# Kernel optimization log

Measured on AMD Instinct MI355X. Metric: run time of the kernel, lower is better.

Reference implementation:

```python
import jax, jax.numpy as jnp
import numpy as np

B, S, H = 2, 2048, 2048
NH, NKV = 16, 4
HD = H // NH          # 128
N_REP = NH // NKV     # 4


def _rotate_half(x):
    x1, x2 = x[..., : x.shape[-1] // 2], x[..., x.shape[-1] // 2 :]
    return jnp.concatenate((-x2, x1), axis=-1)


def setup_inputs() -> dict:
    key = jax.random.key(0)
    ks = jax.random.split(key, 5)
    hidden_states = jax.random.normal(ks[0], (B, S, H), dtype=jnp.float32)
    # true rotary tables [max_seq_len, head_dim]
    inv_freq = 1.0 / (10000.0 ** (np.arange(0, HD, 2, dtype=np.float32) / HD))
    t = np.arange(S, dtype=np.float32)
    freqs = np.outer(t, inv_freq)                    # [S, HD/2]
    emb = np.concatenate([freqs, freqs], axis=-1)    # [S, HD]
    cos = jnp.asarray(np.cos(emb))
    sin = jnp.asarray(np.sin(emb))
    Wq = jax.random.normal(ks[1], (H, NH * HD), dtype=jnp.float32) * 0.02
    Wk = jax.random.normal(ks[2], (H, NKV * HD), dtype=jnp.float32) * 0.02
    Wv = jax.random.normal(ks[3], (H, NKV * HD), dtype=jnp.float32) * 0.02
    Wo = jax.random.normal(ks[4], (NH * HD, H), dtype=jnp.float32) * 0.02
    attention_mask = jnp.ones((B, S), dtype=jnp.float32)  # 1 = keep
    return {"hidden_states": hidden_states, "cos": cos, "sin": sin,
            "Wq": Wq, "Wk": Wk, "Wv": Wv, "Wo": Wo,
            "attention_mask": attention_mask}


def reference(hidden_states, cos, sin, Wq, Wk, Wv, Wo, attention_mask):
    # Decoder self-attention: is_causal=True, use_rope=True, no cache, eval (dropout off).
    x = hidden_states
    b, s, _ = x.shape
    q = jnp.einsum('bsh,hd->bsd', x, Wq).reshape(b, s, NH, HD).transpose(0, 2, 1, 3)   # [b,nh,s,hd]
    k = jnp.einsum('bsh,hd->bsd', x, Wk).reshape(b, s, NKV, HD)
    v = jnp.einsum('bsh,hd->bsd', x, Wv).reshape(b, s, NKV, HD)
    # GQA repeat_kv: each kv head repeated n_rep times contiguously
    k = jnp.repeat(k, N_REP, axis=2).transpose(0, 2, 1, 3)   # [b,nh,s,hd]
    v = jnp.repeat(v, N_REP, axis=2).transpose(0, 2, 1, 3)
    # RoPE
    c = cos[:s][None, None, :, :]
    sn = sin[:s][None, None, :, :]
    q = q * c + _rotate_half(q) * sn
    k = k * c + _rotate_half(k) * sn
    # attention scores
    scores = jnp.einsum('bhqd,bhkd->bhqk', q, k) / jnp.sqrt(jnp.float32(HD))
    neg_inf = jnp.finfo(scores.dtype).min
    causal = jnp.triu(jnp.full((s, s), neg_inf, dtype=scores.dtype), k=1)
    scores = scores + causal[None, None, :, :]
    pad = (1.0 - attention_mask[:, None, None, :].astype(scores.dtype)) * neg_inf
    scores = scores + pad
    attn = jax.nn.softmax(scores.astype(jnp.float32), axis=-1).astype(q.dtype)
    out = jnp.einsum('bhqk,bhkd->bhqd', attn, v)             # [b,nh,s,hd]
    out = out.transpose(0, 2, 1, 3).reshape(b, s, NH * HD)
    return jnp.einsum('bsd,dh->bsh', out, Wo)
```

## Files before the change

### kernel.cpp

```cpp
#include <hip/hip_runtime.h>
#include <hip/hip_bf16.h>


typedef __bf16 bf16;
typedef __bf16 bf16x8 __attribute__((ext_vector_type(8)));
typedef __bf16 bf16x4 __attribute__((ext_vector_type(4)));
typedef float  f32x4  __attribute__((ext_vector_type(4)));

#define MFMA_BF16(a, b, c) __builtin_amdgcn_mfma_f32_16x16x32_bf16((a), (b), (c), 0, 0, 0)

__device__ __forceinline__ void glds16(const bf16* g, char* l) {
  __builtin_amdgcn_global_load_lds((__attribute__((address_space(1))) const void*)g,
                                   (__attribute__((address_space(3))) void*)l, 16, 0, 0);
}

__global__ __launch_bounds__(256) void k_cvt_bf16(const float* __restrict__ in,
                                                  bf16* __restrict__ out, int n4) {
  int i = blockIdx.x * 256 + threadIdx.x;
  if (i < n4) {
    float4 v = ((const float4*)in)[i];
    bf16x4 o;
    o[0] = (bf16)v.x; o[1] = (bf16)v.y; o[2] = (bf16)v.z; o[3] = (bf16)v.w;
    ((bf16x4*)out)[i] = o;
  }
}

__global__ __launch_bounds__(256) void k_transpose_w4(const float* __restrict__ Wq,
                                                      const float* __restrict__ Wk,
                                                      const float* __restrict__ Wv,
                                                      const float* __restrict__ Wo,
                                                      bf16* __restrict__ Wtq,
                                                      bf16* __restrict__ Wtk,
                                                      bf16* __restrict__ Wtv,
                                                      bf16* __restrict__ Wto) {
  int z = blockIdx.z;
  const float* W; bf16* Wt; int N;
  if (z == 0)      { W = Wq; Wt = Wtq; N = 2048; }
  else if (z == 1) { W = Wo; Wt = Wto; N = 2048; }
  else if (z == 2) { W = Wk; Wt = Wtk; N = 512; }
  else             { W = Wv; Wt = Wtv; N = 512; }
  int nb = blockIdx.y * 32;
  if (nb >= N) return;
  __shared__ float tile[32][33];
  int tx = threadIdx.x, ty = threadIdx.y;
  int kb = blockIdx.x * 32;
#pragma unroll
  for (int i = 0; i < 4; ++i)
    tile[ty + i * 8][tx] = W[(size_t)(kb + ty + i * 8) * N + nb + tx];
  __syncthreads();
#pragma unroll
  for (int i = 0; i < 4; ++i)
    Wt[(size_t)(nb + ty + i * 8) * 2048 + kb + tx] = (bf16)tile[tx][ty + i * 8];
}

template <typename OUT>
__device__ void gemm_block(const bf16* __restrict__ A, const bf16* __restrict__ Bt,
                           OUT* __restrict__ C, int K, int ldc,
                           int rbase, int cbase, char* sm,
                           float rope_scl, const float* __restrict__ cosb,
                           const float* __restrict__ sinb,
                           bf16* __restrict__ vtr, int vkv) {
  const int tid = threadIdx.x;
  const int lane = tid & 63, wid = tid >> 6;
  const int l15 = lane & 15, lg = lane >> 4;
  char* Asm = sm;
  char* Bsm = sm + 32768;

  f32x4 acc[2][8];
#pragma unroll
  for (int i = 0; i < 2; ++i)
#pragma unroll
    for (int j = 0; j < 8; ++j)
#pragma unroll
      for (int r = 0; r < 4; ++r) acc[i][j][r] = 0.0f;

  const int ob = wid * 4096 + lane * 16;
  auto stage = [&](int buf, int kb) {
#pragma unroll
    for (int c = 0; c < 4; ++c) {
      int o = ob + c * 1024;
      int r = o >> 7;
      int cc = ((o >> 4) & 7) ^ (r & 7);
      int dst = wid * 4096 + c * 1024 + buf * 16384;
      glds16(A + (size_t)(rbase + r) * K + kb + cc * 8, Asm + dst);
      glds16(Bt + (size_t)(cbase + r) * K + kb + cc * 8, Bsm + dst);
    }
  };

  stage(0, 0);
  __syncthreads();
  const int nk = K >> 6;
  for (int t = 0; t < nk; ++t) {
    if (t + 1 < nk) stage((t + 1) & 1, (t + 1) << 6);
    const char* At  = Asm + (t & 1) * 16384;
    const char* Bti = Bsm + (t & 1) * 16384;
#pragma unroll
    for (int ks = 0; ks < 2; ++ks) {
      bf16x8 a[2], b[8];
#pragma unroll
      for (int rf = 0; rf < 2; ++rf) {
        int r = wid * 32 + rf * 16 + l15;
        int slot = (ks * 4 + lg) ^ (r & 7);
        a[rf] = *(const bf16x8*)(At + r * 128 + slot * 16);
      }
#pragma unroll
      for (int nf = 0; nf < 8; ++nf) {
        int n = nf * 16 + l15;
        int slot = (ks * 4 + lg) ^ (n & 7);
        b[nf] = *(const bf16x8*)(Bti + n * 128 + slot * 16);
      }
#pragma unroll
      for (int rf = 0; rf < 2; ++rf)
#pragma unroll
        for (int nf = 0; nf < 8; ++nf)
          acc[rf][nf] = MFMA_BF16(a[rf], b[nf], acc[rf][nf]);
    }
    __syncthreads();
  }

  if (rope_scl != 0.0f) {
#pragma unroll
    for (int rf = 0; rf < 2; ++rf)
#pragma unroll
      for (int r = 0; r < 4; ++r) {
        int s = (rbase + wid * 32 + rf * 16 + lg * 4 + r) & 2047;
#pragma unroll
        for (int nf = 0; nf < 4; ++nf) {
          int d = nf * 16 + l15;
          float v0 = acc[rf][nf][r], v1 = acc[rf][nf + 4][r];
          float c0 = cosb[s * 128 + d],      c1 = cosb[s * 128 + d + 64];
          float s0 = sinb[s * 128 + d],      s1 = sinb[s * 128 + d + 64];
          acc[rf][nf][r]     = (v0 * c0 - v1 * s0) * rope_scl;
          acc[rf][nf + 4][r] = (v1 * c1 + v0 * s1) * rope_scl;
        }
      }
  }

  if (vtr != nullptr) {
#pragma unroll
    for (int rf = 0; rf < 2; ++rf)
#pragma unroll
      for (int nf = 0; nf < 8; ++nf) {
        int s0 = wid * 32 + rf * 16 + lg * 4;
        int d = nf * 16 + l15;
        bf16x4 pk;
#pragma unroll
        for (int r = 0; r < 4; ++r) pk[r] = (bf16)acc[rf][nf][r];
        *(bf16x4*)(sm + d * 256 + ((s0 * 2) ^ ((d & 15) << 4))) = pk;
      }
    __syncthreads();
    const int b4 = (rbase >> 11) * 4;
    const int scol = rbase & 2047;
    const int so = tid & 15;
#pragma unroll
    for (int i = 0; i < 8; ++i) {
      int d = (tid >> 4) + i * 16;
      bf16x8 v = *(const bf16x8*)(sm + d * 256 + ((so * 16) ^ ((d & 15) << 4)));
      *(bf16x8*)(vtr + (size_t)((b4 + vkv) * 128 + d) * 2048 + scol + so * 8) = v;
    }
    return;
  }

#pragma unroll
  for (int rf = 0; rf < 2; ++rf)
#pragma unroll
    for (int nf = 0; nf < 8; ++nf)
#pragma unroll
      for (int r = 0; r < 4; ++r) {
        int row = rbase + wid * 32 + rf * 16 + lg * 4 + r;
        int col = cbase + nf * 16 + l15;
        C[(size_t)row * ldc + col] = (OUT)acc[rf][nf][r];
      }
}

__global__ __launch_bounds__(256, 2) void k_gemm_qkv(const bf16* __restrict__ X,
                                                     const bf16* __restrict__ Wtq,
                                                     const bf16* __restrict__ Wtk,
                                                     const bf16* __restrict__ Wtv,
                                                     bf16* __restrict__ Q,
                                                     bf16* __restrict__ Ko,
                                                     bf16* __restrict__ Vt,
                                                     const float* __restrict__ cosb,
                                                     const float* __restrict__ sinb,
                                                     float sclq) {
  __shared__ alignas(16) char sm[65536];
  int nb = blockIdx.y;
  int rbase = blockIdx.x * 128;
  if (nb < 16) {
    gemm_block<bf16>(X, Wtq, Q, 2048, 2048, rbase, nb * 128, sm, sclq, cosb, sinb,
                     nullptr, 0);
  } else if (nb < 20) {
    gemm_block<bf16>(X, Wtk, Ko, 2048, 512, rbase, (nb - 16) * 128, sm, 1.0f, cosb, sinb,
                     nullptr, 0);
  } else {
    gemm_block<bf16>(X, Wtv, (bf16*)nullptr, 2048, 512, rbase, (nb - 20) * 128, sm,
                     0.0f, nullptr, nullptr, Vt, nb - 20);
  }
}

__global__ __launch_bounds__(256, 2) void k_gemm_o(const bf16* __restrict__ AO,
                                                   const bf16* __restrict__ Wto,
                                                   float* __restrict__ Out) {
  __shared__ alignas(16) char sm[65536];
  gemm_block<float>(AO, Wto, Out, 2048, 2048, blockIdx.x * 128, blockIdx.y * 128, sm,
                    0.0f, nullptr, nullptr, nullptr, 0);
}

__global__ __launch_bounds__(256, 2) void k_fattn(const bf16* __restrict__ Qg,
                                                  const bf16* __restrict__ Kg,
                                                  const bf16* __restrict__ Vtg,
                                                  bf16* __restrict__ AO) {
  __shared__ alignas(16) char sm[65536];
  const int lane = threadIdx.x & 63, wid = threadIdx.x >> 6;
  const int l15 = lane & 15, lg = lane >> 4;
  const int wg = blockIdx.x;
  const int grp = wg & 7;
  const int b = grp >> 2, kv = grp & 3;
  const int inner = wg >> 3;
  const int h = kv * 4 + (inner & 3);
  const int pair = inner >> 2;
  const int sA = 31 - pair, sB = pair;
  const int nA = sA + 1;
  const int NT = nA + sB + 1;
  const int q0A = sA * 64 + wid * 16, q0B = sB * 64 + wid * 16;

  const bf16 *ks[4], *vs[4];
#pragma unroll
  for (int i = 0; i < 4; ++i) {
    int c = wid * 256 + i * 64 + lane;
    int kr = c >> 4, kcc = (c & 15) ^ (kr & 15);
    ks[i] = Kg + (size_t)(b * 2048 + kr) * 512 + kv * 128 + kcc * 8;
    int vr = c >> 3, vcc = (c & 7) ^ (vr & 7);
    vs[i] = Vtg + (size_t)((b * 4 + kv) * 128 + vr) * 2048 + vcc * 8;
  }

  auto stage = [&](int t) {
    if (t >= NT) return;
    int kb = ((t < nA) ? t : t - nA) << 6;
    char* base = sm + (t & 1) * 32768 + wid * 4096;
#pragma unroll
    for (int i = 0; i < 4; ++i) {
      glds16(ks[i] + (size_t)kb * 512, base + i * 1024);
      glds16(vs[i] + kb, base + 16384 + i * 1024);
    }
  };

  bf16x8 qf[4];
  f32x4 o[8];
  float mrun, lrun;

  auto loadQ = [&](int q0) {
#pragma unroll
    for (int kf = 0; kf < 4; ++kf)
      qf[kf] = *(const bf16x8*)(Qg + (size_t)(b * 2048 + q0 + l15) * 2048 + h * 128 + kf * 32 + lg * 8);
  };
  auto resetS = [&]() {
#pragma unroll
    for (int j = 0; j < 8; ++j)
#pragma unroll
      for (int r = 0; r < 4; ++r) o[j][r] = 0.0f;
    mrun = -3e38f; lrun = 0.0f;
  };

  auto tile = [&](int t, int kb, int q0, bool diag) {
    stage(t + 1);
    const char* Kt = sm + (t & 1) * 32768;
    const char* Vt = Kt + 16384;

    f32x4 sa[4];
#pragma unroll
    for (int j = 0; j < 4; ++j)
#pragma unroll
      for (int r = 0; r < 4; ++r) sa[j][r] = 0.0f;
    __builtin_amdgcn_s_setprio(1);
#pragma unroll
    for (int kf = 0; kf < 4; ++kf) {
      int slot = (kf * 4 + lg) ^ l15;
#pragma unroll
      for (int nf = 0; nf < 4; ++nf) {
        bf16x8 bk = *(const bf16x8*)(Kt + (nf * 16 + l15) * 256 + slot * 16);
        sa[nf] = MFMA_BF16(bk, qf[kf], sa[nf]);
      }
    }
    __builtin_amdgcn_s_setprio(0);

    if (diag) {
      const int qi = q0 + l15;
#pragma unroll
      for (int nf = 0; nf < 4; ++nf)
#pragma unroll
        for (int r = 0; r < 4; ++r)
          if (kb + nf * 16 + lg * 4 + r > qi) sa[nf][r] = -3e38f;
    }

    float mx = sa[0][0];
#pragma unroll
    for (int nf = 0; nf < 4; ++nf)
#pragma unroll
      for (int r = 0; r < 4; ++r) mx = fmaxf(mx, sa[nf][r]);
    mx = fmaxf(mx, __shfl_xor(mx, 16));
    mx = fmaxf(mx, __shfl_xor(mx, 32));
    if (!__all(mx - mrun <= 8.0f)) {
      float mnew = fmaxf(mrun, mx);
      float fac = __builtin_amdgcn_exp2f(mrun - mnew);
      lrun *= fac;
      f32x4 fv;
#pragma unroll
      for (int r = 0; r < 4; ++r) fv[r] = __shfl(fac, lg * 4 + r);
#pragma unroll
      for (int j = 0; j < 8; ++j) o[j] *= fv;
      mrun = mnew;
    }
    float rs = 0.0f;
    uint32_t u0[4], u1[4];
#pragma unroll
    for (int nf = 0; nf < 4; ++nf) {
      float p0 = __builtin_amdgcn_exp2f(sa[nf][0] - mrun);
      float p1 = __builtin_amdgcn_exp2f(sa[nf][1] - mrun);
      float p2 = __builtin_amdgcn_exp2f(sa[nf][2] - mrun);
      float p3 = __builtin_amdgcn_exp2f(sa[nf][3] - mrun);
      rs += (p0 + p1) + (p2 + p3);
      asm("v_cvt_pk_bf16_f32 %0, %1, %2" : "=v"(u0[nf]) : "v"(p0), "v"(p1));
      asm("v_cvt_pk_bf16_f32 %0, %1, %2" : "=v"(u1[nf]) : "v"(p2), "v"(p3));
    }
    rs += __shfl_xor(rs, 16);
    rs += __shfl_xor(rs, 32);
    lrun += rs;

    uint32_t quad[4][4];
#pragma unroll
    for (int nf = 0; nf < 4; ++nf) {
      uint32_t x0 = (uint32_t)__shfl_xor((int)u0[nf], 16);
      uint32_t x1 = (uint32_t)__shfl_xor((int)u1[nf], 16);
      bool ev = (lg & 1) == 0;
      quad[nf][0] = ev ? u0[nf] : x0;
      quad[nf][1] = ev ? u1[nf] : x1;
      quad[nf][2] = ev ? x0 : u0[nf];
      quad[nf][3] = ev ? x1 : u1[nf];
    }
    union UV { uint32_t u[4]; bf16x8 v; } pa0, pa1;
#pragma unroll
    for (int i = 0; i < 4; ++i) {
      uint32_t s0 = (lg & 1) ? quad[0][i] : quad[1][i];
      uint32_t r0 = (uint32_t)__shfl_xor((int)s0, 32);
      pa0.u[i] = (lg == 0) ? quad[0][i] : (lg == 3) ? quad[1][i] : r0;
      uint32_t s1 = (lg & 1) ? quad[2][i] : quad[3][i];
      uint32_t r1 = (uint32_t)__shfl_xor((int)s1, 32);
      pa1.u[i] = (lg == 0) ? quad[2][i] : (lg == 3) ? quad[3][i] : r1;
    }

    __builtin_amdgcn_s_setprio(1);
#pragma unroll
    for (int nf2 = 0; nf2 < 8; ++nf2) {
      int d = nf2 * 16 + l15;
      bf16x8 vb0 = *(const bf16x8*)(Vt + d * 128 + ((lg ^ (d & 7)) * 16));
      o[nf2] = MFMA_BF16(pa0.v, vb0, o[nf2]);
      bf16x8 vb1 = *(const bf16x8*)(Vt + d * 128 + (((4 + lg) ^ (d & 7)) * 16));
      o[nf2] = MFMA_BF16(pa1.v, vb1, o[nf2]);
    }
    __builtin_amdgcn_s_setprio(0);
    __syncthreads();
  };

  auto epi = [&](int q0) {
    f32x4 linv;
#pragma unroll
    for (int r = 0; r < 4; ++r) linv[r] = 1.0f / __shfl(lrun, lg * 4 + r);
#pragma unroll
    for (int j = 0; j < 8; ++j)
#pragma unroll
      for (int r = 0; r < 4; ++r) {
        size_t row = (size_t)(b * 2048 + q0 + lg * 4 + r);
        AO[row * 2048 + h * 128 + j * 16 + l15] = (bf16)(o[j][r] * linv[r]);
      }
  };

  stage(0);
  __syncthreads();

  loadQ(q0A); resetS();
  for (int t = 0; t < nA; ++t) tile(t, t << 6, q0A, t == nA - 1);
  epi(q0A);

  loadQ(q0B); resetS();
  for (int t = nA; t < NT; ++t) tile(t, (t - nA) << 6, q0B, t == NT - 1);
  epi(q0B);
}

extern "C" void kernel_launch(void* const* d_in, const int* in_sizes, int n_in,
                              void* d_out, int out_size, void* d_ws, size_t ws_size,
                              hipStream_t stream) {
  const float* hs   = (const float*)d_in[0];
  const float* cosb = (const float*)d_in[1];
  const float* sinb = (const float*)d_in[2];
  const float* Wq   = (const float*)d_in[3];
  const float* Wk   = (const float*)d_in[4];
  const float* Wv   = (const float*)d_in[5];
  const float* Wo   = (const float*)d_in[6];
  float* Out = (float*)d_out;

  char* ws = (char*)d_ws;
  size_t off = 0;
  auto alloc = [&](size_t bytes) { char* p = ws + off; off += bytes; return p; };
  bf16* Xbf = (bf16*)alloc((size_t)4096 * 2048 * 2);
  bf16* Wtq = (bf16*)alloc((size_t)2048 * 2048 * 2);
  bf16* Wtk = (bf16*)alloc((size_t)512 * 2048 * 2);
  bf16* Wtv = (bf16*)alloc((size_t)512 * 2048 * 2);
  bf16* Wto = (bf16*)alloc((size_t)2048 * 2048 * 2);
  bf16* Qb  = (bf16*)alloc((size_t)4096 * 2048 * 2);
  bf16* Kb  = (bf16*)alloc((size_t)4096 * 512 * 2);
  bf16* Vtb = (bf16*)alloc((size_t)4096 * 512 * 2);
  bf16* AO  = (bf16*)alloc((size_t)4096 * 2048 * 2);

  const float SCLQ = 0.08838834764831845f * 1.4426950408889634f;

  dim3 tb(32, 8);
  k_cvt_bf16<<<8192, 256, 0, stream>>>(hs, Xbf, 2097152);
  k_transpose_w4<<<dim3(64, 64, 4), tb, 0, stream>>>(Wq, Wk, Wv, Wo, Wtq, Wtk, Wtv, Wto);
  k_gemm_qkv<<<dim3(32, 24), 256, 0, stream>>>(Xbf, Wtq, Wtk, Wtv, Qb, Kb, Vtb,
                                               cosb, sinb, SCLQ);
  k_fattn<<<512, 256, 0, stream>>>(Qb, Kb, Vtb, AO);
  k_gemm_o<<<dim3(32, 16), 256, 0, stream>>>(AO, Wto, Out);
}
```

Measured before the change: 212.6 us.

## Rewrite flash attention with 32x32 MFMA and 128-row query strips

Rewrites the attention kernel around 32x32x16 bf16 MFMAs. Each wave now owns 32 query rows, and each workgroup processes one 128-row strip instead of a pair of 64-row strips. S is computed as K·Q transposed, so row statistics need only one cross-half shuffle, and the epilogue writes packed bf16x4 stores. This removes the paired balancing scheme, so the blocks with long strips and the blocks with short strips now differ in work. The larger per-wave accumulators raise register pressure, and waves skip compute on tiles beyond their causal range while still joining the barriers.

```diff
diff --git a/kernel.cpp b/kernel.cpp
--- a/kernel.cpp
+++ b/kernel.cpp
@@ -6,8 +6,10 @@
 typedef __bf16 bf16x8 __attribute__((ext_vector_type(8)));
 typedef __bf16 bf16x4 __attribute__((ext_vector_type(4)));
 typedef float  f32x4  __attribute__((ext_vector_type(4)));
+typedef float  f32x16 __attribute__((ext_vector_type(16)));
 
 #define MFMA_BF16(a, b, c) __builtin_amdgcn_mfma_f32_16x16x32_bf16((a), (b), (c), 0, 0, 0)
+#define MFMA32(a, b, c)    __builtin_amdgcn_mfma_f32_32x32x16_bf16((a), (b), (c), 0, 0, 0)
 
 __device__ __forceinline__ void glds16(const bf16* g, char* l) {
   __builtin_amdgcn_global_load_lds((__attribute__((address_space(1))) const void*)g,
@@ -212,17 +214,15 @@
                                                   bf16* __restrict__ AO) {
   __shared__ alignas(16) char sm[65536];
   const int lane = threadIdx.x & 63, wid = threadIdx.x >> 6;
-  const int l15 = lane & 15, lg = lane >> 4;
+  const int l31 = lane & 31, lh = lane >> 5;
   const int wg = blockIdx.x;
   const int grp = wg & 7;
   const int b = grp >> 2, kv = grp & 3;
   const int inner = wg >> 3;
-  const int h = kv * 4 + (inner & 3);
-  const int pair = inner >> 2;
-  const int sA = 31 - pair, sB = pair;
-  const int nA = sA + 1;
-  const int NT = nA + sB + 1;
-  const int q0A = sA * 64 + wid * 16, q0B = sB * 64 + wid * 16;
+  const int head = kv * 4 + (inner & 3);
+  const int strip = 15 - (inner >> 2);
+  const int q0w = strip * 128 + wid * 32;
+  const int nt = 2 * (strip + 1);
 
   const bf16 *ks[4], *vs[4];
 #pragma unroll
@@ -233,10 +233,9 @@
     int vr = c >> 3, vcc = (c & 7) ^ (vr & 7);
     vs[i] = Vtg + (size_t)((b * 4 + kv) * 128 + vr) * 2048 + vcc * 8;
   }
-
   auto stage = [&](int t) {
-    if (t >= NT) return;
-    int kb = ((t < nA) ? t : t - nA) << 6;
+    if (t >= nt) return;
+    int kb = t << 6;
     char* base = sm + (t & 1) * 32768 + wid * 4096;
 #pragma unroll
     for (int i = 0; i < 4; ++i) {
@@ -245,146 +244,133 @@
     }
   };
 
-  bf16x8 qf[4];
-  f32x4 o[8];
-  float mrun, lrun;
-
-  auto loadQ = [&](int q0) {
-#pragma unroll
-    for (int kf = 0; kf < 4; ++kf)
-      qf[kf] = *(const bf16x8*)(Qg + (size_t)(b * 2048 + q0 + l15) * 2048 + h * 128 + kf * 32 + lg * 8);
-  };
-  auto resetS = [&]() {
-#pragma unroll
-    for (int j = 0; j < 8; ++j)
-#pragma unroll
-      for (int r = 0; r < 4; ++r) o[j][r] = 0.0f;
-    mrun = -3e38f; lrun = 0.0f;
-  };
-
-  auto tile = [&](int t, int kb, int q0, bool diag) {
+  bf16x8 qf[8];
+#pragma unroll
+  for (int st = 0; st < 8; ++st)
+    qf[st] = *(const bf16x8*)(Qg + (size_t)(b * 2048 + q0w + l31) * 2048 +
+                              head * 128 + st * 16 + lh * 8);
+
+  f32x16 o[4];
+#pragma unroll
+  for (int j = 0; j < 4; ++j)
+#pragma unroll
+    for (int r = 0; r < 16; ++r) o[j][r] = 0.0f;
+  float mrun = -3e38f, lrun = 0.0f;
+
+  stage(0);
+  __syncthreads();
+
+  for (int t = 0; t < nt; ++t) {
+    const int kb = t << 6;
     stage(t + 1);
     const char* Kt = sm + (t & 1) * 32768;
     const char* Vt = Kt + 16384;
 
-    f32x4 sa[4];
-#pragma unroll
-    for (int j = 0; j < 4; ++j)
-#pragma unroll
-      for (int r = 0; r < 4; ++r) sa[j][r] = 0.0f;
-    __builtin_amdgcn_s_setprio(1);
-#pragma unroll
-    for (int kf = 0; kf < 4; ++kf) {
-      int slot = (kf * 4 + lg) ^ l15;
-#pragma unroll
-      for (int nf = 0; nf < 4; ++nf) {
-        bf16x8 bk = *(const bf16x8*)(Kt + (nf * 16 + l15) * 256 + slot * 16);
-        sa[nf] = MFMA_BF16(bk, qf[kf], sa[nf]);
-      }
-    }
-    __builtin_amdgcn_s_setprio(0);
-
-    if (diag) {
-      const int qi = q0 + l15;
-#pragma unroll
-      for (int nf = 0; nf < 4; ++nf)
-#pragma unroll
-        for (int r = 0; r < 4; ++r)
-          if (kb + nf * 16 + lg * 4 + r > qi) sa[nf][r] = -3e38f;
-    }
-
-    float mx = sa[0][0];
-#pragma unroll
-    for (int nf = 0; nf < 4; ++nf)
-#pragma unroll
-      for (int r = 0; r < 4; ++r) mx = fmaxf(mx, sa[nf][r]);
-    mx = fmaxf(mx, __shfl_xor(mx, 16));
-    mx = fmaxf(mx, __shfl_xor(mx, 32));
-    if (!__all(mx - mrun <= 8.0f)) {
-      float mnew = fmaxf(mrun, mx);
-      float fac = __builtin_amdgcn_exp2f(mrun - mnew);
-      lrun *= fac;
-      f32x4 fv;
-#pragma unroll
-      for (int r = 0; r < 4; ++r) fv[r] = __shfl(fac, lg * 4 + r);
-#pragma unroll
-      for (int j = 0; j < 8; ++j) o[j] *= fv;
-      mrun = mnew;
-    }
-    float rs = 0.0f;
-    uint32_t u0[4], u1[4];
-#pragma unroll
-    for (int nf = 0; nf < 4; ++nf) {
-      float p0 = __builtin_amdgcn_exp2f(sa[nf][0] - mrun);
-      float p1 = __builtin_amdgcn_exp2f(sa[nf][1] - mrun);
-      float p2 = __builtin_amdgcn_exp2f(sa[nf][2] - mrun);
-      float p3 = __builtin_amdgcn_exp2f(sa[nf][3] - mrun);
-      rs += (p0 + p1) + (p2 + p3);
-      asm("v_cvt_pk_bf16_f32 %0, %1, %2" : "=v"(u0[nf]) : "v"(p0), "v"(p1));
-      asm("v_cvt_pk_bf16_f32 %0, %1, %2" : "=v"(u1[nf]) : "v"(p2), "v"(p3));
-    }
-    rs += __shfl_xor(rs, 16);
-    rs += __shfl_xor(rs, 32);
-    lrun += rs;
-
-    uint32_t quad[4][4];
-#pragma unroll
-    for (int nf = 0; nf < 4; ++nf) {
-      uint32_t x0 = (uint32_t)__shfl_xor((int)u0[nf], 16);
-      uint32_t x1 = (uint32_t)__shfl_xor((int)u1[nf], 16);
-      bool ev = (lg & 1) == 0;
-      quad[nf][0] = ev ? u0[nf] : x0;
-      quad[nf][1] = ev ? u1[nf] : x1;
-      quad[nf][2] = ev ? x0 : u0[nf];
-      quad[nf][3] = ev ? x1 : u1[nf];
-    }
-    union UV { uint32_t u[4]; bf16x8 v; } pa0, pa1;
-#pragma unroll
-    for (int i = 0; i < 4; ++i) {
-      uint32_t s0 = (lg & 1) ? quad[0][i] : quad[1][i];
-      uint32_t r0 = (uint32_t)__shfl_xor((int)s0, 32);
-      pa0.u[i] = (lg == 0) ? quad[0][i] : (lg == 3) ? quad[1][i] : r0;
-      uint32_t s1 = (lg & 1) ? quad[2][i] : quad[3][i];
-      uint32_t r1 = (uint32_t)__shfl_xor((int)s1, 32);
-      pa1.u[i] = (lg == 0) ? quad[2][i] : (lg == 3) ? quad[3][i] : r1;
-    }
-
-    __builtin_amdgcn_s_setprio(1);
-#pragma unroll
-    for (int nf2 = 0; nf2 < 8; ++nf2) {
-      int d = nf2 * 16 + l15;
-      bf16x8 vb0 = *(const bf16x8*)(Vt + d * 128 + ((lg ^ (d & 7)) * 16));
-      o[nf2] = MFMA_BF16(pa0.v, vb0, o[nf2]);
-      bf16x8 vb1 = *(const bf16x8*)(Vt + d * 128 + (((4 + lg) ^ (d & 7)) * 16));
-      o[nf2] = MFMA_BF16(pa1.v, vb1, o[nf2]);
-    }
-    __builtin_amdgcn_s_setprio(0);
+    if (kb <= q0w + 31) {
+      f32x16 sa[2];
+#pragma unroll
+      for (int j = 0; j < 2; ++j)
+#pragma unroll
+        for (int r = 0; r < 16; ++r) sa[j][r] = 0.0f;
+      __builtin_amdgcn_s_setprio(1);
+#pragma unroll
+      for (int st = 0; st < 8; ++st) {
+#pragma unroll
+        for (int kt = 0; kt < 2; ++kt) {
+          int row = kt * 32 + l31;
+          int slot = (st * 2 + lh) ^ (row & 15);
+          bf16x8 ka = *(const bf16x8*)(Kt + row * 256 + slot * 16);
+          sa[kt] = MFMA32(ka, qf[st], sa[kt]);
+        }
+      }
+      __builtin_amdgcn_s_setprio(0);
+
+      if (kb + 63 > q0w) {
+        const int qi = q0w + l31;
+#pragma unroll
+        for (int kt = 0; kt < 2; ++kt)
+#pragma unroll
+          for (int r = 0; r < 16; ++r) {
+            int kg = kb + kt * 32 + (r & 3) + 8 * (r >> 2) + 4 * lh;
+            if (kg > qi) sa[kt][r] = -3e38f;
+          }
+      }
+
+      float mx = sa[0][0];
+#pragma unroll
+      for (int kt = 0; kt < 2; ++kt)
+#pragma unroll
+        for (int r = 0; r < 16; ++r) mx = fmaxf(mx, sa[kt][r]);
+      mx = fmaxf(mx, __shfl_xor(mx, 32));
+      if (!__all(mx - mrun <= 8.0f)) {
+        float mnew = fmaxf(mrun, mx);
+        float fac = __builtin_amdgcn_exp2f(mrun - mnew);
+        lrun *= fac;
+#pragma unroll
+        for (int j = 0; j < 4; ++j)
+#pragma unroll
+          for (int r = 0; r < 16; ++r) o[j][r] *= fac;
+        mrun = mnew;
+      }
+
+      union UV { uint32_t u[4]; bf16x8 v; } frag[4];
+      float rs = 0.0f;
+#pragma unroll
+      for (int kt = 0; kt < 2; ++kt) {
+        float pe[16];
+#pragma unroll
+        for (int r = 0; r < 16; ++r) {
+          pe[r] = __builtin_amdgcn_exp2f(sa[kt][r] - mrun);
+          rs += pe[r];
+        }
+        uint32_t c[8];
+#pragma unroll
+        for (int g = 0; g < 8; ++g)
+          asm("v_cvt_pk_bf16_f32 %0, %1, %2" : "=v"(c[g]) : "v"(pe[2 * g]), "v"(pe[2 * g + 1]));
+#pragma unroll
+        for (int f = 0; f < 2; ++f) {
+          int bi = f * 4;
+          uint32_t va = lh ? c[bi + 0] : c[bi + 2];
+          uint32_t ra = (uint32_t)__shfl_xor((int)va, 32);
+          uint32_t vb = lh ? c[bi + 1] : c[bi + 3];
+          uint32_t rb = (uint32_t)__shfl_xor((int)vb, 32);
+          UV& fr = frag[kt * 2 + f];
+          fr.u[0] = lh ? ra : c[bi + 0];
+          fr.u[1] = lh ? rb : c[bi + 1];
+          fr.u[2] = lh ? c[bi + 2] : ra;
+          fr.u[3] = lh ? c[bi + 3] : rb;
+        }
+      }
+      rs += __shfl_xor(rs, 32);
+      lrun += rs;
+
+      __builtin_amdgcn_s_setprio(1);
+#pragma unroll
+      for (int dt = 0; dt < 4; ++dt) {
+        int row = dt * 32 + l31;
+#pragma unroll
+        for (int kf = 0; kf < 4; ++kf) {
+          int slot = (kf * 2 + lh) ^ (row & 7);
+          bf16x8 va = *(const bf16x8*)(Vt + row * 128 + slot * 16);
+          o[dt] = MFMA32(va, frag[kf].v, o[dt]);
+        }
+      }
+      __builtin_amdgcn_s_setprio(0);
+    }
     __syncthreads();
-  };
-
-  auto epi = [&](int q0) {
-    f32x4 linv;
-#pragma unroll
-    for (int r = 0; r < 4; ++r) linv[r] = 1.0f / __shfl(lrun, lg * 4 + r);
-#pragma unroll
-    for (int j = 0; j < 8; ++j)
-#pragma unroll
-      for (int r = 0; r < 4; ++r) {
-        size_t row = (size_t)(b * 2048 + q0 + lg * 4 + r);
-        AO[row * 2048 + h * 128 + j * 16 + l15] = (bf16)(o[j][r] * linv[r]);
-      }
-  };
-
-  stage(0);
-  __syncthreads();
-
-  loadQ(q0A); resetS();
-  for (int t = 0; t < nA; ++t) tile(t, t << 6, q0A, t == nA - 1);
-  epi(q0A);
-
-  loadQ(q0B); resetS();
-  for (int t = nA; t < NT; ++t) tile(t, (t - nA) << 6, q0B, t == NT - 1);
-  epi(q0B);
+  }
+
+  float linv = 1.0f / lrun;
+  bf16* aop = AO + (size_t)(b * 2048 + q0w + l31) * 2048 + head * 128;
+#pragma unroll
+  for (int dt = 0; dt < 4; ++dt)
+#pragma unroll
+    for (int g = 0; g < 4; ++g) {
+      bf16x4 pk;
+#pragma unroll
+      for (int j = 0; j < 4; ++j) pk[j] = (bf16)(o[dt][4 * g + j] * linv);
+      *(bf16x4*)(aop + dt * 32 + g * 8 + lh * 4) = pk;
+    }
 }
 
 extern "C" void kernel_launch(void* const* d_in, const int* in_sizes, int n_in,
```

Result: faster. 200.5 us (-5.7%).
